# Performance work log

Hardware: AMD Instinct MI355X
Metric: run time of the kernel (lower is better)

Reference implementation:

```python
import jax, jax.numpy as jnp
import numpy as np

B, S, H, V, C = 32, 512, 256, 50000, 5
NUM_LAYERS, WINDOW = 2, 2


def setup_inputs() -> dict:
    key = jax.random.key(0)
    ks = jax.random.split(key, 24)
    std = 0.1  # matches nn.init.normal_(p, 0, 0.1)
    n = lambda k, shp: jax.random.normal(k, shp, dtype=jnp.float32) * std
    u = lambda k, shp: -0.05 + jax.random.uniform(k, shp, dtype=jnp.float32) * 0.1
    return {
        "input_sentences": jax.random.randint(ks[0], (B, S), 0, V),
        "sentences_length": jax.random.randint(ks[1], (B,), 1, S),
        "hh0": u(ks[2], (B, S, H)),
        "cs0": u(ks[3], (B, S, H)),
        "embed": n(ks[4], (V, H)),
        # stacked word-gate weights, gate order: i, l, r, f, s, output, u
        "W_lr": n(ks[5], (7, H, 2 * H)),
        "W_c": n(ks[6], (7, H, H)),
        "W_x": n(ks[7], (7, H, H)),
        "W_g": n(ks[8], (7, H, H)),
        "gate_bias": n(ks[9], (7, H)),
        # sentence-state gates
        "W_fg_g": n(ks[10], (H, H)),
        "W_fg_h": n(ks[11], (H, H)),
        "W_fgi_g": n(ks[12], (H, H)),
        "W_fgi_h": n(ks[13], (H, H)),
        "W_og_g": n(ks[14], (H, H)),
        "W_og_h": n(ks[15], (H, H)),
        "b_fg": n(ks[16], (H,)),
        "b_fgi": n(ks[17], (H,)),
        # output head
        "W1": n(ks[18], (H, 2 * H)),
        "b1": n(ks[19], (H,)),
        "Wout": n(ks[20], (C, H)),
        "bout": n(ks[21], (C,)),
    }


def _before_sum(x, window):
    # sum of right-shifted (zero-padded at front) copies, shifts 1..window
    out = jnp.zeros_like(x)
    for s in range(1, window + 1):
        out = out + jnp.pad(x[:, :-s], ((0, 0), (s, 0), (0, 0)))
    return out


def _after_sum(x, window):
    out = jnp.zeros_like(x)
    for s in range(1, window + 1):
        out = out + jnp.pad(x[:, s:], ((0, 0), (0, s), (0, 0)))
    return out


def _slstm_step(hh, cs, sv, scs, wv, W_lr, W_c, W_x, W_g, gate_bias,
                W_fg_g, W_fg_h, W_fgi_g, W_fgi_h, W_og_g, W_og_h, b_fg, b_fgi):
    avg_hh = hh.mean(axis=1)                                   # [B,H]
    f_hat_g = jax.nn.sigmoid(sv @ W_fg_g.T + avg_hh @ W_fg_h.T + b_fg)
    # NOTE: original code (faithfully) uses output_gate_bias here, not output_gate_g_bias
    og_g = jax.nn.sigmoid(sv @ W_og_g.T + avg_hh @ W_og_h.T + gate_bias[5])
    f_hat_g_i = jax.nn.sigmoid((sv @ W_fgi_g.T)[:, None] + hh @ W_fgi_h.T + b_fgi)
    scores = jax.nn.softmax(f_hat_g_i, axis=2)                 # over hidden dim
    new_scs = jax.nn.softmax(f_hat_g, axis=1) * scs + (scores * cs).sum(axis=1)
    new_sv = og_g * jnp.tanh(new_scs)

    hb = _before_sum(hh, WINDOW)
    ha = _after_sum(hh, WINDOW)
    cb = _before_sum(cs, WINDOW)
    ca = _after_sum(cs, WINDOW)
    ba = jnp.concatenate([hb, ha], axis=-1)                    # [B,S,2H]

    # all 7 gate pre-activations at once: [B,S,7,H]
    pre = (jnp.einsum('bsk,ghk->bsgh', ba, W_lr)
           + jnp.einsum('bsk,ghk->bsgh', hh, W_c)
           + jnp.einsum('bsk,ghk->bsgh', wv, W_x)
           + (jnp.einsum('bk,ghk->bgh', new_sv, W_g) + gate_bias)[:, None])

    g5 = jax.nn.sigmoid(pre[..., :5, :])                       # i,l,r,f,s
    b_, s_ = g5.shape[:2]
    # joint softmax over the concatenated 5*H gate vector (as in torch cat+softmax)
    g5 = jax.nn.softmax(g5.reshape(b_, s_, -1), axis=-1).reshape(b_, s_, 5, -1)
    i_t, l_t, r_t, f_t, s_t = (g5[..., k, :] for k in range(5))
    og = jax.nn.sigmoid(pre[..., 5, :])
    u_g = jnp.tanh(pre[..., 6, :])

    new_cs = l_t * cb + f_t * cs + r_t * ca + s_t * scs[:, None] + i_t * u_g
    new_hh = og * jnp.tanh(new_cs)
    return new_hh, new_cs, new_sv, new_scs


def reference(input_sentences, sentences_length, hh0, cs0, embed,
              W_lr, W_c, W_x, W_g, gate_bias,
              W_fg_g, W_fg_h, W_fgi_g, W_fgi_h, W_og_g, W_og_h, b_fg, b_fgi,
              W1, b1, Wout, bout):
    wv = embed[input_sentences]                                # [B,S,H]
    hh, cs = hh0, cs0
    sv, scs = hh0.mean(axis=1), cs0.mean(axis=1)
    for _ in range(NUM_LAYERS):
        hh, cs, sv, scs = _slstm_step(hh, cs, sv, scs, wv,
                                      W_lr, W_c, W_x, W_g, gate_bias,
                                      W_fg_g, W_fg_h, W_fgi_g, W_fgi_h,
                                      W_og_g, W_og_h, b_fg, b_fgi)
    avg_hh = hh.mean(axis=1)
    conc = jnp.concatenate([avg_hh, sv], axis=1) @ W1.T + b1
    fc = conc @ Wout.T + bout
    return jax.nn.log_softmax(fc, axis=1), sv
```

## Files before the change

kernel.cpp:

```cpp
#include <hip/hip_runtime.h>
#include <stdint.h>
#include <math.h>

#define B_   32
#define S_   512
#define H_   256
#define M_   (B_*S_)
#define KBIG 1024
#define NB   1792
#define C_   5

typedef __bf16 bf16;
typedef __bf16 bf16x8 __attribute__((ext_vector_type(8)));
typedef float  floatx4 __attribute__((ext_vector_type(4)));

__device__ __forceinline__ float sigm(float x){ return 1.f/(1.f+expf(-x)); }

__global__ void wcomb_k(const float* __restrict__ Wlr, const float* __restrict__ Wc,
                        const float* __restrict__ Wx, bf16* __restrict__ WT){
    int n = blockIdx.x;
    int g = n >> 8, h = n & 255;
    int k4 = threadIdx.x * 4;
    const float* src;
    if (k4 < 512)      src = Wlr + ((size_t)(g*256 + h))*512 + k4;
    else if (k4 < 768) src = Wc  + ((size_t)(g*256 + h))*256 + (k4 - 512);
    else               src = Wx  + ((size_t)(g*256 + h))*256 + (k4 - 768);
    float4 v = *(const float4*)src;
    bf16 o[4] = {(bf16)v.x,(bf16)v.y,(bf16)v.z,(bf16)v.w};
    *(uint2*)&WT[(size_t)n*KBIG + k4] = *(uint2*)o;
}

__global__ void cvtw_k(const float* __restrict__ a, bf16* __restrict__ o){
    int i4 = (blockIdx.x*256 + threadIdx.x)*4;
    float4 v = *(const float4*)(a + i4);
    bf16 t[4] = {(bf16)v.x,(bf16)v.y,(bf16)v.z,(bf16)v.w};
    *(uint2*)(o + i4) = *(uint2*)t;
}

__global__ void gather_k(const int* __restrict__ idx, const float* __restrict__ embed,
                         bf16* __restrict__ wv){
    int i4 = (blockIdx.x*256 + threadIdx.x)*4;
    int m = i4 >> 8, h = i4 & 255;
    float4 v = *(const float4*)(embed + (size_t)idx[m]*H_ + h);
    bf16 o[4] = {(bf16)v.x,(bf16)v.y,(bf16)v.z,(bf16)v.w};
    *(uint2*)(wv + (size_t)m*H_ + h) = *(uint2*)o;
}

__global__ void mean1_k(const float* __restrict__ x, float* __restrict__ part){
    int b = blockIdx.x, c = blockIdx.y, h = threadIdx.x;
    const float* p = x + ((size_t)b*S_ + c*32)*H_ + h;
    float s = 0.f;
    #pragma unroll 8
    for (int t=0;t<32;t++) s += p[(size_t)t*H_];
    part[((size_t)b*16 + c)*H_ + h] = s;
}
__global__ void mean2_k(const float* __restrict__ part, float* __restrict__ out){
    int b = blockIdx.x, h = threadIdx.x;
    float s = 0.f;
    #pragma unroll
    for (int c=0;c<16;c++) s += part[((size_t)b*16 + c)*H_ + h];
    out[b*H_ + h] = s * (1.f/512.f);
}

__global__ void buildx_k(const float* __restrict__ hh, const bf16* __restrict__ wv,
                         bf16* __restrict__ X){
    int m = blockIdx.x, h = threadIdx.x;
    int s = m & (S_-1);
    size_t base = (size_t)m*H_ + h;
    float hb = (s>=1    ? hh[base - H_] : 0.f) + (s>=2    ? hh[base - 2*H_] : 0.f);
    float ha = (s<=S_-2 ? hh[base + H_] : 0.f) + (s<=S_-3 ? hh[base + 2*H_] : 0.f);
    bf16* xr = X + (size_t)m*KBIG;
    xr[h]     = (bf16)hb;
    xr[256+h] = (bf16)ha;
    xr[512+h] = (bf16)hh[base];
    xr[768+h] = wv[base];
}

__global__ void mv5_k(const float* __restrict__ sv, const float* __restrict__ avg,
    const float* __restrict__ Wfg_g, const float* __restrict__ Wfg_h,
    const float* __restrict__ Wog_g, const float* __restrict__ Wog_h,
    const float* __restrict__ Wfgi_g, float* __restrict__ res){
    int j = blockIdx.x, b = blockIdx.y, h = threadIdx.x;
    const float* vec = (j==1 || j==3) ? avg + b*H_ : sv + b*H_;
    const float* W   = (j==0)?Wfg_g:(j==1)?Wfg_h:(j==2)?Wog_g:(j==3)?Wog_h:Wfgi_g;
    __shared__ float v[H_];
    v[h] = vec[h]; __syncthreads();
    const float* w = W + (size_t)h*H_;
    float d = 0.f;
    for (int k=0;k<H_;k++) d += v[k]*w[k];
    res[((size_t)b*5 + j)*H_ + h] = d;
}
__global__ void comb_k(const float* __restrict__ res, const float* __restrict__ b_fg,
                       const float* __restrict__ gbias, const float* __restrict__ b_fgi,
                       float* __restrict__ fhg, float* __restrict__ ogg,
                       float* __restrict__ svg){
    int b = blockIdx.x, h = threadIdx.x;
    const float* r = res + (size_t)b*5*H_;
    fhg[b*H_+h] = sigm(r[h] + r[H_+h] + b_fg[h]);
    ogg[b*H_+h] = sigm(r[2*H_+h] + r[3*H_+h] + gbias[5*H_+h]);
    svg[b*H_+h] = r[4*H_+h] + b_fgi[h];
}

template<int EPI>
__global__ __launch_bounds__(256)
void mgemm_k(const bf16* __restrict__ A, const bf16* __restrict__ BT,
             bf16* __restrict__ C, const float* __restrict__ gt,
             int Kdim, int lda, int ldb, int ldc){
    __shared__ alignas(16) bf16 lsA[128*32];
    __shared__ alignas(16) bf16 lsB[128*32];
    int tid  = threadIdx.x;
    int m0 = blockIdx.y * 128, n0 = blockIdx.x * 128;
    int wave = tid >> 6, lane = tid & 63;
    int wm = (wave & 1) * 64, wn = (wave >> 1) * 64;
    int lrow = lane & 15, quad = lane >> 4;

    floatx4 zero = {0.f,0.f,0.f,0.f};
    floatx4 acc[4][4];
    #pragma unroll
    for (int i=0;i<4;i++)
        #pragma unroll
        for (int j=0;j<4;j++) acc[i][j] = zero;

    int srow = tid >> 2;
    int scol = (tid & 3) * 8;
    const bf16* Abase = A  + (size_t)(m0 + srow)*lda + scol;
    const bf16* Bbase = BT + (size_t)(n0 + srow)*ldb + scol;

    for (int k0 = 0; k0 < Kdim; k0 += 32){
        __syncthreads();
        *(uint4*)&lsA[srow*32 + scol]      = *(const uint4*)(Abase + k0);
        *(uint4*)&lsA[(64+srow)*32 + scol] = *(const uint4*)(Abase + (size_t)64*lda + k0);
        *(uint4*)&lsB[srow*32 + scol]      = *(const uint4*)(Bbase + k0);
        *(uint4*)&lsB[(64+srow)*32 + scol] = *(const uint4*)(Bbase + (size_t)64*ldb + k0);
        __syncthreads();
        bf16x8 af[4], bfr[4];
        #pragma unroll
        for (int mi=0;mi<4;mi++) af[mi]  = *(const bf16x8*)&lsA[(wm+mi*16+lrow)*32 + quad*8];
        #pragma unroll
        for (int ni=0;ni<4;ni++) bfr[ni] = *(const bf16x8*)&lsB[(wn+ni*16+lrow)*32 + quad*8];
        #pragma unroll
        for (int mi=0;mi<4;mi++)
            #pragma unroll
            for (int ni=0;ni<4;ni++)
                acc[mi][ni] = __builtin_amdgcn_mfma_f32_16x16x32_bf16(af[mi], bfr[ni], acc[mi][ni], 0, 0, 0);
    }

    #pragma unroll
    for (int mi=0;mi<4;mi++)
        #pragma unroll
        for (int ni=0;ni<4;ni++){
            int row = m0 + wm + mi*16 + quad*4;
            int col = n0 + wn + ni*16 + lrow;
            #pragma unroll
            for (int r=0;r<4;r++){
                float v = acc[mi][ni][r];
                if (EPI) v += gt[(size_t)((row+r)>>9)*NB + col];
                C[(size_t)(row+r)*ldc + col] = (bf16)v;
            }
        }
}

__global__ void scorep_k(const bf16* __restrict__ fgih, const float* __restrict__ svg,
                         const float* __restrict__ cs, float* __restrict__ part){
    int chunk = blockIdx.x, b = blockIdx.y, h = threadIdx.x;
    __shared__ float r[256];
    float sw = svg[b*H_+h];
    float acc = 0.f;
    for (int j=0;j<16;j++){
        int m = b*S_ + chunk*16 + j;
        float e = expf(sigm(sw + (float)fgih[(size_t)m*H_ + h]));
        r[h] = e; __syncthreads();
        for (int off=128; off; off>>=1){ if (h<off) r[h] += r[h+off]; __syncthreads(); }
        acc += (e / r[0]) * cs[(size_t)m*H_ + h];
        __syncthreads();
    }
    part[((size_t)b*32 + chunk)*H_ + h] = acc;
}

__global__ void newscs_k(const float* __restrict__ part, const float* __restrict__ fhg,
                         const float* __restrict__ ogg, const float* __restrict__ scs_in,
                         float* __restrict__ scs_out, float* __restrict__ sv_out){
    int b = blockIdx.x, h = threadIdx.x;
    __shared__ float r[256];
    float dot = 0.f;
    #pragma unroll 8
    for (int c=0;c<32;c++) dot += part[((size_t)b*32+c)*H_ + h];
    float e = expf(fhg[b*H_+h]);
    r[h] = e; __syncthreads();
    for (int off=128; off; off>>=1){ if (h<off) r[h] += r[h+off]; __syncthreads(); }
    float ns = (e / r[0]) * scs_in[b*H_+h] + dot;
    scs_out[b*H_+h] = ns;
    sv_out[b*H_+h]  = ogg[b*H_+h] * tanhf(ns);
}

__global__ void gterm_k(const float* __restrict__ svn, const float* __restrict__ Wg,
                        const float* __restrict__ gbias, float* __restrict__ gt){
    int g = blockIdx.x, b = blockIdx.y, h = threadIdx.x;
    __shared__ float s[H_];
    s[h] = svn[b*H_+h]; __syncthreads();
    const float* w = Wg + ((size_t)g*H_ + h)*H_;
    float d = 0.f;
    for (int k=0;k<H_;k++) d += s[k]*w[k];
    gt[(size_t)b*NB + g*H_ + h] = d + gbias[g*H_+h];
}

__global__ void gates_k(const bf16* __restrict__ pre, const float* __restrict__ cs_in,
                        const float* __restrict__ scs_in,
                        float* __restrict__ hh_out, float* __restrict__ cs_out){
    int m = blockIdx.x, h = threadIdx.x, b = m >> 9, s = m & (S_-1);
    __shared__ float r[256];
    const bf16* row = pre + (size_t)m*NB;
    float pg[7];
    #pragma unroll
    for (int g=0; g<7; ++g) pg[g] = (float)row[g*H_ + h];
    float ex[5]; float loc = 0.f;
    #pragma unroll
    for (int g=0; g<5; ++g){ ex[g] = expf(sigm(pg[g])); loc += ex[g]; }
    r[h] = loc; __syncthreads();
    for (int off=128; off; off>>=1){ if (h<off) r[h] += r[h+off]; __syncthreads(); }
    float inv = 1.f / r[0];
    size_t i = (size_t)m*H_ + h;
    float cb = (s>=1    ? cs_in[i - H_] : 0.f) + (s>=2    ? cs_in[i - 2*H_] : 0.f);
    float ca = (s<=S_-2 ? cs_in[i + H_] : 0.f) + (s<=S_-3 ? cs_in[i + 2*H_] : 0.f);
    float nc = ex[1]*inv*cb + ex[3]*inv*cs_in[i] + ex[2]*inv*ca
             + ex[4]*inv*scs_in[b*H_+h] + ex[0]*inv*tanhf(pg[6]);
    cs_out[i] = nc;
    hh_out[i] = sigm(pg[5]) * tanhf(nc);
}

__global__ void head_k(const float* __restrict__ avgh, const float* __restrict__ sv,
                       const float* __restrict__ W1, const float* __restrict__ b1,
                       const float* __restrict__ Wout, const float* __restrict__ bout,
                       float* __restrict__ out){
    int b = blockIdx.x, t = threadIdx.x;
    __shared__ float conc[H_];
    __shared__ float fc[8];
    const float* wr = W1 + (size_t)t*512;
    float d = b1[t];
    for (int k=0;k<H_;k++) d += avgh[b*H_+k]*wr[k];
    for (int k=0;k<H_;k++) d += sv[b*H_+k]*wr[256+k];
    conc[t] = d;
    __syncthreads();
    if (t < C_){
        const float* wo = Wout + (size_t)t*H_;
        float s = bout[t];
        for (int i=0;i<H_;i++) s += conc[i]*wo[i];
        fc[t] = s;
    }
    __syncthreads();
    if (t == 0){
        float mx = fc[0];
        for (int c=1;c<C_;c++) mx = fmaxf(mx, fc[c]);
        float se = 0.f;
        for (int c=0;c<C_;c++) se += expf(fc[c]-mx);
        float lse = mx + logf(se);
        for (int c=0;c<C_;c++) out[b*C_+c] = fc[c]-lse;
    }
    out[B_*C_ + b*H_ + t] = sv[b*H_+t];
}

extern "C" void kernel_launch(void* const* d_in, const int* in_sizes, int n_in,
                              void* d_out, int out_size, void* d_ws, size_t ws_size,
                              hipStream_t stream){
    const int*   idx    = (const int*)d_in[0];
    const float* hh0    = (const float*)d_in[2];
    const float* cs0    = (const float*)d_in[3];
    const float* embed  = (const float*)d_in[4];
    const float* Wlr    = (const float*)d_in[5];
    const float* Wc     = (const float*)d_in[6];
    const float* Wx     = (const float*)d_in[7];
    const float* Wg     = (const float*)d_in[8];
    const float* gbias  = (const float*)d_in[9];
    const float* Wfg_g  = (const float*)d_in[10];
    const float* Wfg_h  = (const float*)d_in[11];
    const float* Wfgi_g = (const float*)d_in[12];
    const float* Wfgi_h = (const float*)d_in[13];
    const float* Wog_g  = (const float*)d_in[14];
    const float* Wog_h  = (const float*)d_in[15];
    const float* b_fg   = (const float*)d_in[16];
    const float* b_fgi  = (const float*)d_in[17];
    const float* W1     = (const float*)d_in[18];
    const float* b1     = (const float*)d_in[19];
    const float* Wout   = (const float*)d_in[20];
    const float* bout   = (const float*)d_in[21];

    uint8_t* p = (uint8_t*)d_ws;
    auto alloc = [&](size_t bytes)->void*{ void* r=(void*)p; p += (bytes + 255) & ~(size_t)255; return r; };
    bf16*  WT    = (bf16*)alloc((size_t)NB*KBIG*2);
    bf16*  WfgiT = (bf16*)alloc((size_t)H_*H_*2);
    bf16*  X     = (bf16*)alloc((size_t)M_*KBIG*2);
    bf16*  wv    = (bf16*)alloc((size_t)M_*H_*2);
    bf16*  pre   = (bf16*)alloc((size_t)M_*NB*2);
    bf16*  fgih  = (bf16*)alloc((size_t)M_*H_*2);
    float* hhA = (float*)alloc((size_t)M_*H_*4);
    float* csA = (float*)alloc((size_t)M_*H_*4);
    float* hhB = (float*)alloc((size_t)M_*H_*4);
    float* csB = (float*)alloc((size_t)M_*H_*4);
    float* mpart= (float*)alloc((size_t)B_*16*H_*4);
    float* part = (float*)alloc((size_t)B_*32*H_*4);
    float* res5 = (float*)alloc((size_t)B_*5*H_*4);
    float* avgh = (float*)alloc(B_*H_*4);
    float* fhg  = (float*)alloc(B_*H_*4);
    float* ogg  = (float*)alloc(B_*H_*4);
    float* svg  = (float*)alloc(B_*H_*4);
    float* svP0 = (float*)alloc(B_*H_*4);
    float* svP1 = (float*)alloc(B_*H_*4);
    float* scP0 = (float*)alloc(B_*H_*4);
    float* scP1 = (float*)alloc(B_*H_*4);
    float* gt   = (float*)alloc((size_t)B_*NB*4);

    wcomb_k <<<NB,          256, 0, stream>>>(Wlr, Wc, Wx, WT);
    cvtw_k  <<<(H_*H_)/1024,256, 0, stream>>>(Wfgi_h, WfgiT);
    gather_k<<<(M_*H_)/1024,256, 0, stream>>>(idx, embed, wv);
    mean1_k <<<dim3(B_,16), 256, 0, stream>>>(hh0, mpart);
    mean2_k <<<B_,          256, 0, stream>>>(mpart, svP0);
    mean1_k <<<dim3(B_,16), 256, 0, stream>>>(cs0, mpart);
    mean2_k <<<B_,          256, 0, stream>>>(mpart, scP0);

    const float *hin = hh0, *cin = cs0;
    float *hout = hhA, *cout = csA;
    float *svin = svP0, *scin = scP0, *svout = svP1, *scout = scP1;

    for (int l=0; l<2; ++l){
        const float* avgp;
        if (l == 0){
            avgp = svin;
        } else {
            mean1_k<<<dim3(B_,16), 256, 0, stream>>>(hin, mpart);
            mean2_k<<<B_,          256, 0, stream>>>(mpart, avgh);
            avgp = avgh;
        }
        mv5_k   <<<dim3(5,B_), 256, 0, stream>>>(svin, avgp, Wfg_g, Wfg_h, Wog_g,
                                                 Wog_h, Wfgi_g, res5);
        comb_k  <<<B_, 256, 0, stream>>>(res5, b_fg, gbias, b_fgi, fhg, ogg, svg);
        buildx_k<<<M_, 256, 0, stream>>>(hin, wv, X);
        mgemm_k<0><<<dim3(2,128), 256, 0, stream>>>(X+512, WfgiT, fgih, nullptr,
                                                    H_, KBIG, H_, H_);
        scorep_k<<<dim3(32,B_), 256, 0, stream>>>(fgih, svg, cin, part);
        newscs_k<<<B_, 256, 0, stream>>>(part, fhg, ogg, scin, scout, svout);
        gterm_k <<<dim3(7,B_), 256, 0, stream>>>(svout, Wg, gbias, gt);
        mgemm_k<1><<<dim3(14,128), 256, 0, stream>>>(X, WT, pre, gt,
                                                     KBIG, KBIG, KBIG, NB);
        gates_k <<<M_, 256, 0, stream>>>(pre, cin, scin, hout, cout);
        hin = hout; cin = cout;
        hout = (l==0) ? hhB : hhA;
        cout = (l==0) ? csB : csA;
        float* q;
        q = svin; svin = svout; svout = q;
        q = scin; scin = scout; scout = q;
    }
    mean1_k<<<dim3(B_,16), 256, 0, stream>>>(hin, mpart);
    mean2_k<<<B_,          256, 0, stream>>>(mpart, avgh);
    head_k <<<B_, 256, 0, stream>>>(avgh, svin, W1, b1, Wout, bout, (float*)d_out);
}
```

Before: 592.8 us.

## Use direct global-to-LDS loads in GEMM and wave-level reductions in softmax kernels

The GEMM tile loads now use global_load_lds to write straight into shared memory instead of staging through registers. scorep_k and gates_k replace block-wide shared-memory tree reductions, which need many __syncthreads, with one wave per row and shuffle-xor reductions. gates_k now handles four rows per block, so the grid shrinks accordingly. The direct-to-LDS path depends on the layout mapping of lanes to LDS addresses being correct, and the GEMM still has no double buffering.

```diff
diff --git a/kernel.cpp b/kernel.cpp
--- a/kernel.cpp
+++ b/kernel.cpp
@@ -15,6 +15,12 @@
 typedef float  floatx4 __attribute__((ext_vector_type(4)));
 
 __device__ __forceinline__ float sigm(float x){ return 1.f/(1.f+expf(-x)); }
+
+__device__ __forceinline__ void gl16(const bf16* g, bf16* l){
+    __builtin_amdgcn_global_load_lds(
+        (const __attribute__((address_space(1))) unsigned int*)g,
+        (__attribute__((address_space(3))) unsigned int*)l, 16, 0, 0);
+}
 
 __global__ void wcomb_k(const float* __restrict__ Wlr, const float* __restrict__ Wc,
                         const float* __restrict__ Wx, bf16* __restrict__ WT){
@@ -125,13 +131,17 @@
     int scol = (tid & 3) * 8;
     const bf16* Abase = A  + (size_t)(m0 + srow)*lda + scol;
     const bf16* Bbase = BT + (size_t)(n0 + srow)*ldb + scol;
+    bf16* dA0 = &lsA[srow*32 + scol];
+    bf16* dA1 = &lsA[(64+srow)*32 + scol];
+    bf16* dB0 = &lsB[srow*32 + scol];
+    bf16* dB1 = &lsB[(64+srow)*32 + scol];
 
     for (int k0 = 0; k0 < Kdim; k0 += 32){
         __syncthreads();
-        *(uint4*)&lsA[srow*32 + scol]      = *(const uint4*)(Abase + k0);
-        *(uint4*)&lsA[(64+srow)*32 + scol] = *(const uint4*)(Abase + (size_t)64*lda + k0);
-        *(uint4*)&lsB[srow*32 + scol]      = *(const uint4*)(Bbase + k0);
-        *(uint4*)&lsB[(64+srow)*32 + scol] = *(const uint4*)(Bbase + (size_t)64*ldb + k0);
+        gl16(Abase + k0,                     dA0);
+        gl16(Abase + (size_t)64*lda + k0,    dA1);
+        gl16(Bbase + k0,                     dB0);
+        gl16(Bbase + (size_t)64*ldb + k0,    dB1);
         __syncthreads();
         bf16x8 af[4], bfr[4];
         #pragma unroll
@@ -162,19 +172,30 @@
 
 __global__ void scorep_k(const bf16* __restrict__ fgih, const float* __restrict__ svg,
                          const float* __restrict__ cs, float* __restrict__ part){
-    int chunk = blockIdx.x, b = blockIdx.y, h = threadIdx.x;
-    __shared__ float r[256];
-    float sw = svg[b*H_+h];
-    float acc = 0.f;
-    for (int j=0;j<16;j++){
-        int m = b*S_ + chunk*16 + j;
-        float e = expf(sigm(sw + (float)fgih[(size_t)m*H_ + h]));
-        r[h] = e; __syncthreads();
-        for (int off=128; off; off>>=1){ if (h<off) r[h] += r[h+off]; __syncthreads(); }
-        acc += (e / r[0]) * cs[(size_t)m*H_ + h];
-        __syncthreads();
-    }
-    part[((size_t)b*32 + chunk)*H_ + h] = acc;
+    int chunk = blockIdx.x, b = blockIdx.y;
+    int tid = threadIdx.x, wave = tid >> 6, lane = tid & 63;
+    __shared__ float acc4[4][256];
+    float sw[4], acc[4] = {0.f,0.f,0.f,0.f};
+    #pragma unroll
+    for (int j=0;j<4;j++) sw[j] = svg[b*H_ + lane + 64*j];
+    for (int t=wave; t<16; t+=4){
+        int m = b*S_ + chunk*16 + t;
+        const bf16* fr = fgih + (size_t)m*H_;
+        float e[4], loc = 0.f;
+        #pragma unroll
+        for (int j=0;j<4;j++){ e[j] = expf(sigm(sw[j] + (float)fr[lane+64*j])); loc += e[j]; }
+        #pragma unroll
+        for (int off=32; off; off>>=1) loc += __shfl_xor(loc, off, 64);
+        float inv = 1.f/loc;
+        const float* cr = cs + (size_t)m*H_;
+        #pragma unroll
+        for (int j=0;j<4;j++) acc[j] += e[j]*inv*cr[lane+64*j];
+    }
+    #pragma unroll
+    for (int j=0;j<4;j++) acc4[wave][lane+64*j] = acc[j];
+    __syncthreads();
+    part[((size_t)b*32 + chunk)*H_ + tid] =
+        acc4[0][tid] + acc4[1][tid] + acc4[2][tid] + acc4[3][tid];
 }
 
 __global__ void newscs_k(const float* __restrict__ part, const float* __restrict__ fhg,
@@ -207,25 +228,37 @@
 __global__ void gates_k(const bf16* __restrict__ pre, const float* __restrict__ cs_in,
                         const float* __restrict__ scs_in,
                         float* __restrict__ hh_out, float* __restrict__ cs_out){
-    int m = blockIdx.x, h = threadIdx.x, b = m >> 9, s = m & (S_-1);
-    __shared__ float r[256];
+    int tid = threadIdx.x, wave = tid >> 6, lane = tid & 63;
+    int m = blockIdx.x*4 + wave;
+    int b = m >> 9, s = m & (S_-1);
     const bf16* row = pre + (size_t)m*NB;
-    float pg[7];
-    #pragma unroll
-    for (int g=0; g<7; ++g) pg[g] = (float)row[g*H_ + h];
-    float ex[5]; float loc = 0.f;
-    #pragma unroll
-    for (int g=0; g<5; ++g){ ex[g] = expf(sigm(pg[g])); loc += ex[g]; }
-    r[h] = loc; __syncthreads();
-    for (int off=128; off; off>>=1){ if (h<off) r[h] += r[h+off]; __syncthreads(); }
-    float inv = 1.f / r[0];
-    size_t i = (size_t)m*H_ + h;
-    float cb = (s>=1    ? cs_in[i - H_] : 0.f) + (s>=2    ? cs_in[i - 2*H_] : 0.f);
-    float ca = (s<=S_-2 ? cs_in[i + H_] : 0.f) + (s<=S_-3 ? cs_in[i + 2*H_] : 0.f);
-    float nc = ex[1]*inv*cb + ex[3]*inv*cs_in[i] + ex[2]*inv*ca
-             + ex[4]*inv*scs_in[b*H_+h] + ex[0]*inv*tanhf(pg[6]);
-    cs_out[i] = nc;
-    hh_out[i] = sigm(pg[5]) * tanhf(nc);
+    float ex[4][5], og[4], u[4];
+    float loc = 0.f;
+    #pragma unroll
+    for (int j=0;j<4;j++){
+        int h = lane + 64*j;
+        #pragma unroll
+        for (int g=0; g<5; ++g){
+            float e = expf(sigm((float)row[g*H_ + h]));
+            ex[j][g] = e; loc += e;
+        }
+        og[j] = sigm((float)row[5*H_ + h]);
+        u[j]  = tanhf((float)row[6*H_ + h]);
+    }
+    #pragma unroll
+    for (int off=32; off; off>>=1) loc += __shfl_xor(loc, off, 64);
+    float inv = 1.f / loc;
+    #pragma unroll
+    for (int j=0;j<4;j++){
+        int h = lane + 64*j;
+        size_t i = (size_t)m*H_ + h;
+        float cb = (s>=1    ? cs_in[i - H_] : 0.f) + (s>=2    ? cs_in[i - 2*H_] : 0.f);
+        float ca = (s<=S_-2 ? cs_in[i + H_] : 0.f) + (s<=S_-3 ? cs_in[i + 2*H_] : 0.f);
+        float nc = ex[j][1]*inv*cb + ex[j][3]*inv*cs_in[i] + ex[j][2]*inv*ca
+                 + ex[j][4]*inv*scs_in[b*H_+h] + ex[j][0]*inv*u[j];
+        cs_out[i] = nc;
+        hh_out[i] = og[j] * tanhf(nc);
+    }
 }
 
 __global__ void head_k(const float* __restrict__ avgh, const float* __restrict__ sv,
@@ -341,7 +374,7 @@
         gterm_k <<<dim3(7,B_), 256, 0, stream>>>(svout, Wg, gbias, gt);
         mgemm_k<1><<<dim3(14,128), 256, 0, stream>>>(X, WT, pre, gt,
                                                      KBIG, KBIG, KBIG, NB);
-        gates_k <<<M_, 256, 0, stream>>>(pre, cin, scin, hout, cout);
+        gates_k <<<M_/4, 256, 0, stream>>>(pre, cin, scin, hout, cout);
         hin = hout; cin = cout;
         hout = (l==0) ? hhB : hhA;
         cout = (l==0) ? csB : csA;
```

Result: faster. 571.8 us (-3.5%).
